# Kernel optimization log

Measured on AMD Instinct MI355X. Metric: run time of the kernel, lower is better.

Reference implementation:

```python
import jax, jax.numpy as jnp
import numpy as np

H = 2048      # hidden_size
K = 16        # n_memory_tokens
NQ = K + 2    # extraction queries (+halt, +value)
NH = 4        # extraction heads
HD = H // NH  # head dim = 512
FFN = 2 * H   # ffn_mult=2
MAXE = 128    # memory buffer capacity (full -> eviction path)
B, S = 4, 4096
EPS = 1e-6


def setup_inputs() -> dict:
    key = jax.random.key(0)
    ks = jax.random.split(key, 20)
    r = lambda i, shape, s=0.02: jax.random.normal(ks[i], shape, jnp.float32) * s
    return {
        "hidden_states": jax.random.normal(ks[0], (B, S, H), jnp.float32),
        "buf_entries": jax.random.normal(ks[1], (MAXE, H), jnp.float32),
        "buf_priorities": jax.random.uniform(ks[2], (MAXE,), jnp.float32),
        "queries": r(3, (NQ, H)),
        "Wq": r(4, (H, H)), "Wk": r(5, (H, H)), "Wv": r(6, (H, H)), "Wo": r(7, (H, H)),
        "ln_w": jnp.ones((H,), jnp.float32),
        "Wgate": r(8, (FFN, H)), "Wup": r(9, (FFN, H)), "Wdown": r(10, (H, FFN)),
        "Wp": r(11, (1, H)), "bp": jnp.full((1,), 0.5, jnp.float32),
        "Wh": r(12, (1, H)), "bh": jnp.full((1,), 1.0, jnp.float32),
        "V1": r(13, (H, 2 * H)), "b1": jnp.zeros((H,), jnp.float32),
        "V2": r(14, (H // 4, H)), "b2": jnp.zeros((H // 4,), jnp.float32),
        "V3": jnp.zeros((1, H // 4), jnp.float32), "b3": jnp.zeros((1,), jnp.float32),
    }


def reference(hidden_states, buf_entries, buf_priorities, queries,
              Wq, Wk, Wv, Wo, ln_w, Wgate, Wup, Wdown,
              Wp, bp, Wh, bh, V1, b1, V2, b2, V3, b3):
    b = hidden_states.shape[0]
    # --- cross-attention: NQ learned queries attend over hidden states ---
    q = (queries @ Wq.T).reshape(NQ, NH, HD)               # queries shared across batch
    k = (hidden_states @ Wk.T).reshape(b, -1, NH, HD)      # (b, s, h, d)
    v = (hidden_states @ Wv.T).reshape(b, -1, NH, HD)
    scores = jnp.einsum('qhd,bshd->bhqs', q, k) / jnp.sqrt(jnp.float32(HD))
    attn = jax.nn.softmax(scores, axis=-1)
    out = jnp.einsum('bhqs,bshd->bqhd', attn, v).reshape(b, NQ, H)
    extracted = out @ Wo.T
    memory_raw = extracted[:, :K]            # (b, K, H)
    confidence_vec = extracted[:, K]         # (b, H)
    value_vec = extracted[:, K + 1]          # (b, H)
    # --- RMSNorm + SwiGLU FFN residual (dropout = identity in eval) ---
    ms = jnp.mean(memory_raw * memory_raw, axis=-1, keepdims=True)
    xn = memory_raw * jax.lax.rsqrt(ms + EPS) * ln_w
    ffn = (jax.nn.silu(xn @ Wgate.T) * (xn @ Wup.T)) @ Wdown.T
    memory = memory_raw + ffn
    # --- heads ---
    priority = jax.nn.sigmoid(memory @ Wp.T + bp)[..., 0]          # (b, K)
    confidence = jax.nn.sigmoid(confidence_vec @ Wh.T + bh)[..., 0]  # (b,)
    value_input = jnp.concatenate([value_vec, hidden_states[:, -1, :]], axis=-1)
    h1 = jax.nn.silu(value_input @ V1.T + b1)
    h2 = jax.nn.silu(h1 @ V2.T + b2)
    value = (h2 @ V3.T + b3)[..., 0]                               # (b,)
    # --- MemoryBuffer.store with full buffer: sequential priority eviction ---
    # (torch loops K times with argmin().item() host syncs; lax.scan preserves
    #  the sequential compare-and-replace semantics in one fused program)
    vecs = jax.lax.stop_gradient(memory[0])     # store detaches; uses batch 0
    pris = jax.lax.stop_gradient(priority[0])

    def step(carry, xp):
        ent, pr = carry
        vec, p = xp
        idx = jnp.argmin(pr)
        take = p > pr[idx]
        ent = ent.at[idx].set(jnp.where(take, vec, ent[idx]))
        pr = pr.at[idx].set(jnp.where(take, p, pr[idx]))
        return (ent, pr), None

    (new_entries, new_priorities), _ = jax.lax.scan(step, (buf_entries, buf_priorities), (vecs, pris))
    return memory, priority, confidence, value, new_entries, new_priorities
```

## Files before the change

### kernel.cpp

```cpp
#include <hip/hip_runtime.h>

#define SS    4096
#define HH    2048
#define NQQ   18
#define QH    72
#define SCALE_F 0.044194173824159216f

#define OUT_MEM     0
#define OUT_PRI     131072
#define OUT_CONF    131136
#define OUT_VAL     131140
#define OUT_ENT     131144
#define OUT_NEWPRI  393288

typedef float  f32x4  __attribute__((ext_vector_type(4)));
typedef __bf16 bf16x8 __attribute__((ext_vector_type(8)));

#define DEVFN static __device__ __forceinline__

DEVFN bf16x8 pack8(f32x4 lo, f32x4 hi){
  bf16x8 r;
  #pragma unroll
  for (int i = 0; i < 4; i++){ r[i] = (__bf16)lo[i]; r[i+4] = (__bf16)hi[i]; }
  return r;
}
DEVFN float siluf(float x){ return x / (1.f + expf(-x)); }
DEVFN float block_sum(float v, float* sb){
  #pragma unroll
  for (int o = 32; o > 0; o >>= 1) v += __shfl_xor(v, o);
  int wid = threadIdx.x >> 6, lane = threadIdx.x & 63;
  if (lane == 0) sb[wid] = v;
  __syncthreads();
  v = sb[0] + sb[1] + sb[2] + sb[3];
  __syncthreads();
  return v;
}

template<int MF, int KC, bool HSEL>
__global__ __launch_bounds__(256) void gemm_bt(
    const __bf16* __restrict__ A, int Kf,
    const float* __restrict__ B0, float* __restrict__ C0,
    const float* __restrict__ B1, float* __restrict__ C1,
    int N)
{
  constexpr int Mp = 16 * MF;
  const int lane = threadIdx.x & 63, w = threadIdx.x >> 6;
  const int n0 = blockIdx.x * 64 + w * 16;
  const int k0 = blockIdx.y * KC * 32;
  const float* B = blockIdx.z ? B1 : B0;
  float* Cp      = blockIdx.z ? C1 : C0;
  const __bf16* aBase = A + (HSEL ? (long)(n0 >> 9) * Mp * Kf : 0)
                          + (long)(lane & 15) * Kf + k0 + 8 * (lane >> 4);
  const float* bBase = B + (long)(n0 + (lane & 15)) * Kf + k0 + 8 * (lane >> 4);
  f32x4 acc[MF];
  #pragma unroll
  for (int m = 0; m < MF; m++) acc[m] = (f32x4)(0.f);
  #pragma unroll 4
  for (int c = 0; c < KC; c++){
    f32x4 lo = *reinterpret_cast<const f32x4*>(bBase + c * 32);
    f32x4 hi = *reinterpret_cast<const f32x4*>(bBase + c * 32 + 4);
    bf16x8 bb = pack8(lo, hi);
    #pragma unroll
    for (int m = 0; m < MF; m++){
      bf16x8 aa = *reinterpret_cast<const bf16x8*>(aBase + (long)m * 16 * Kf + c * 32);
      acc[m] = __builtin_amdgcn_mfma_f32_16x16x32_bf16(aa, bb, acc[m], 0, 0, 0);
    }
  }
  float* cp = Cp + (long)blockIdx.y * Mp * N;
  int row0 = 4 * (lane >> 4), col = n0 + (lane & 15);
  #pragma unroll
  for (int m = 0; m < MF; m++)
    #pragma unroll
    for (int r = 0; r < 4; r++)
      cp[(long)(m * 16 + row0 + r) * N + col] = acc[m][r];
}

template<int MF, int KC>
__global__ __launch_bounds__(256) void gemm_abnat(
    const __bf16* __restrict__ A, long aBatch, int aStride,
    const float* __restrict__ Bn, long bBatch,
    float* __restrict__ Cp, long cBatch,
    int N)
{
  constexpr int Mp = 16 * MF;
  const int lane = threadIdx.x & 63, w = threadIdx.x >> 6;
  const int z = blockIdx.z;
  const int n0 = blockIdx.x * 64 + w * 16;
  const int k0 = blockIdx.y * KC * 32;
  const __bf16* aBase = A + z * aBatch + (long)(lane & 15) * aStride + k0 + 8 * (lane >> 4);
  const float* bBase = Bn + z * bBatch + (long)(k0 + 8 * (lane >> 4)) * N + n0 + (lane & 15);
  f32x4 acc[MF];
  #pragma unroll
  for (int m = 0; m < MF; m++) acc[m] = (f32x4)(0.f);
  #pragma unroll 2
  for (int c = 0; c < KC; c++){
    const float* bp = bBase + (long)c * 32 * N;
    bf16x8 bb;
    #pragma unroll
    for (int j = 0; j < 8; j++) bb[j] = (__bf16)bp[(long)j * N];
    #pragma unroll
    for (int m = 0; m < MF; m++){
      bf16x8 aa = *reinterpret_cast<const bf16x8*>(aBase + (long)m * 16 * aStride + c * 32);
      acc[m] = __builtin_amdgcn_mfma_f32_16x16x32_bf16(aa, bb, acc[m], 0, 0, 0);
    }
  }
  float* cp = Cp + z * cBatch + (long)blockIdx.y * Mp * N;
  int row0 = 4 * (lane >> 4), col = n0 + (lane & 15);
  #pragma unroll
  for (int m = 0; m < MF; m++)
    #pragma unroll
    for (int r = 0; r < 4; r++)
      cp[(long)(m * 16 + row0 + r) * N + col] = acc[m][r];
}

template<int KC>
__global__ __launch_bounds__(256) void gemm_pass1(
    const float* __restrict__ hs, const __bf16* __restrict__ qk,
    float* __restrict__ Sp)
{
  const int lane = threadIdx.x & 63, w = threadIdx.x >> 6;
  const int b = blockIdx.z;
  const int s0 = blockIdx.x * 64 + w * 16;
  const int k0 = blockIdx.y * KC * 32;
  const float* aBase = hs + ((long)b * SS + s0 + (lane & 15)) * HH + k0 + 8 * (lane >> 4);
  const __bf16* bBase = qk + (long)(lane & 15) * HH + k0 + 8 * (lane >> 4);
  f32x4 acc[5];
  #pragma unroll
  for (int n = 0; n < 5; n++) acc[n] = (f32x4)(0.f);
  #pragma unroll 4
  for (int c = 0; c < KC; c++){
    f32x4 lo = *reinterpret_cast<const f32x4*>(aBase + c * 32);
    f32x4 hi = *reinterpret_cast<const f32x4*>(aBase + c * 32 + 4);
    bf16x8 aa = pack8(lo, hi);
    #pragma unroll
    for (int n = 0; n < 5; n++){
      bf16x8 bb = *reinterpret_cast<const bf16x8*>(bBase + (long)n * 16 * HH + c * 32);
      acc[n] = __builtin_amdgcn_mfma_f32_16x16x32_bf16(aa, bb, acc[n], 0, 0, 0);
    }
  }
  float* sp = Sp + ((long)blockIdx.y * 4 + b) * 80 * SS;
  int scol = s0 + 4 * (lane >> 4);
  #pragma unroll
  for (int n = 0; n < 5; n++){
    int qh = n * 16 + (lane & 15);
    *reinterpret_cast<f32x4*>(sp + (long)qh * SS + scol) = acc[n];
  }
}

__global__ void k_prep_qA(const float* __restrict__ queries, __bf16* __restrict__ qA){
  int i = blockIdx.x * 256 + threadIdx.x;
  int r = i >> 11;
  qA[i] = (__bf16)((r < NQQ) ? queries[i] : 0.f);
}
__global__ void k_mkQ2(const float* __restrict__ q_p, __bf16* __restrict__ Q2){
  int i = blockIdx.x * 256 + threadIdx.x;
  int qh = i >> 11, e = i & 2047;
  float v = 0.f;
  if (qh < QH){
    int h = qh / NQQ, qq = qh - h * NQQ;
    if ((e >> 9) == h){
      float s = 0.f;
      #pragma unroll
      for (int y = 0; y < 16; y++) s += q_p[(long)y * 32 * 2048 + qq * 2048 + e];
      v = s * SCALE_F;
    }
  }
  Q2[i] = (__bf16)v;
}
__global__ void k_mkqk(const float* __restrict__ qk_p, __bf16* __restrict__ qk_bf){
  int i = blockIdx.x * 256 + threadIdx.x;
  float s = 0.f;
  #pragma unroll
  for (int y = 0; y < 16; y++) s += qk_p[(long)y * 80 * 2048 + i];
  qk_bf[i] = (__bf16)s;
}
__global__ __launch_bounds__(256) void k_softmax(const float* __restrict__ Sp, __bf16* __restrict__ attn){
  int qh = blockIdx.x, b = blockIdx.y;
  __bf16* arow = attn + ((long)b * 80 + qh) * SS;
  if (qh >= QH){
    #pragma unroll
    for (int it = 0; it < 16; it++) arow[threadIdx.x + 256 * it] = (__bf16)0.f;
    return;
  }
  const float* r0 = Sp + ((long)b * 80 + qh) * SS;
  const long ys = (long)4 * 80 * SS;
  float x[16]; float mx = -1e30f;
  #pragma unroll
  for (int it = 0; it < 16; it++){
    int s = threadIdx.x + 256 * it;
    x[it] = (r0[s] + r0[s + ys]) + (r0[s + 2 * ys] + r0[s + 3 * ys]);
    mx = fmaxf(mx, x[it]);
  }
  __shared__ float sb[8];
  #pragma unroll
  for (int o = 32; o > 0; o >>= 1) mx = fmaxf(mx, __shfl_xor(mx, o));
  int wid = threadIdx.x >> 6, lane = threadIdx.x & 63;
  if (lane == 0) sb[wid] = mx;
  __syncthreads();
  mx = fmaxf(fmaxf(sb[0], sb[1]), fmaxf(sb[2], sb[3]));
  float sum = 0.f;
  #pragma unroll
  for (int it = 0; it < 16; it++){ x[it] = expf(x[it] - mx); sum += x[it]; }
  #pragma unroll
  for (int o = 32; o > 0; o >>= 1) sum += __shfl_xor(sum, o);
  if (lane == 0) sb[4 + wid] = sum;
  __syncthreads();
  sum = sb[4] + sb[5] + sb[6] + sb[7];
  float inv = 1.f / sum;
  #pragma unroll
  for (int it = 0; it < 16; it++) arow[threadIdx.x + 256 * it] = (__bf16)(x[it] * inv);
}
__global__ void k_pack_wv(const float* __restrict__ w_p, __bf16* __restrict__ Apack){
  int i = blockIdx.x * 256 + threadIdx.x;
  int h = i / (80 * 2048);
  int r = (i / 2048) % 80;
  int e = i & 2047;
  float v = 0.f;
  if (r < QH){
    int b = r / NQQ, qq = r - b * NQQ;
    const float* base = w_p + ((long)b * 8 * 80 + (h * NQQ + qq)) * 2048 + e;
    #pragma unroll
    for (int y = 0; y < 8; y++) v += base[(long)y * 80 * 2048];
  }
  Apack[i] = (__bf16)v;
}
__global__ void k_sum_outB(const float* __restrict__ outB_p, __bf16* __restrict__ outB){
  int i = blockIdx.x * 256 + threadIdx.x;
  float s = 0.f;
  #pragma unroll
  for (int y = 0; y < 16; y++) s += outB_p[(long)y * 80 * 2048 + i];
  outB[i] = (__bf16)s;
}
__global__ __launch_bounds__(256) void k_rms(const float* __restrict__ ext_p, const float* __restrict__ ln_w,
                                             const float* __restrict__ hs,
                                             float* __restrict__ extracted, __bf16* __restrict__ xnb,
                                             __bf16* __restrict__ vi){
  int r = blockIdx.x;
  if (r >= 80){
    if (r < 84){
      int b = r - 80;
      const float* src = hs + ((long)b * SS + (SS - 1)) * HH;
      #pragma unroll
      for (int it = 0; it < 8; it++){
        int e = threadIdx.x + 256 * it;
        vi[(long)b * 4096 + 2048 + e] = (__bf16)src[e];
      }
    } else {
      int row = 4 + (r - 84);
      #pragma unroll
      for (int it = 0; it < 16; it++)
        vi[(long)row * 4096 + threadIdx.x + 256 * it] = (__bf16)0.f;
    }
    return;
  }
  float xv[8]; float ss = 0.f;
  #pragma unroll
  for (int it = 0; it < 8; it++){
    int e = threadIdx.x + 256 * it;
    float s = 0.f;
    #pragma unroll
    for (int y = 0; y < 16; y++) s += ext_p[((long)y * 80 + r) * 2048 + e];
    extracted[(long)r * 2048 + e] = s;
    xv[it] = s;
    ss += s * s;
  }
  if (r >= QH) return;
  int b = r / NQQ, qq = r - b * NQQ;
  if (qq < 16){
    __shared__ float sb[4];
    ss = block_sum(ss, sb);
    float inv = 1.f / sqrtf(ss * (1.f / 2048.f) + 1e-6f);
    __bf16* dst = xnb + (long)(b * 16 + qq) * HH;
    #pragma unroll
    for (int it = 0; it < 8; it++){
      int e = threadIdx.x + 256 * it;
      dst[e] = (__bf16)(xv[it] * inv * ln_w[e]);
    }
  } else if (qq == 17){
    #pragma unroll
    for (int it = 0; it < 8; it++){
      int e = threadIdx.x + 256 * it;
      vi[(long)b * 4096 + e] = (__bf16)xv[it];
    }
  }
}
__global__ void k_act(const float* __restrict__ gate_p, const float* __restrict__ up_p,
                      __bf16* __restrict__ hb){
  int i = blockIdx.x * 256 + threadIdx.x;
  float g = 0.f, u = 0.f;
  #pragma unroll
  for (int y = 0; y < 4; y++){
    g += gate_p[(long)y * 64 * 4096 + i];
    u += up_p[(long)y * 64 * 4096 + i];
  }
  hb[i] = (__bf16)(siluf(g) * u);
}
__global__ void k_h1act(const float* __restrict__ h1_p, const float* __restrict__ b1,
                        __bf16* __restrict__ h1s){
  int i = blockIdx.x * 256 + threadIdx.x;
  int r = i >> 11, e = i & 2047;
  float v = 0.f;
  if (r < 4){
    float s = 0.f;
    #pragma unroll
    for (int y = 0; y < 16; y++) s += h1_p[(long)y * 16 * 2048 + i];
    v = siluf(s + b1[e]);
  }
  h1s[i] = (__bf16)v;
}
__global__ __launch_bounds__(256) void k_epilogue(
    const float* __restrict__ extracted, const float* __restrict__ ffn_p,
    const float* __restrict__ h2_p,
    const float* __restrict__ Wp, const float* __restrict__ bp,
    const float* __restrict__ Wh, const float* __restrict__ bh,
    const float* __restrict__ b2, const float* __restrict__ V3, const float* __restrict__ b3,
    float* __restrict__ out)
{
  __shared__ float sb[4];
  int blk = blockIdx.x;
  if (blk < 64){
    int b = blk >> 4, qq = blk & 15;
    const float* ext = extracted + (long)(b * NQQ + qq) * HH;
    float pv = 0.f;
    #pragma unroll
    for (int it = 0; it < 8; it++){
      int e = threadIdx.x + 256 * it;
      float f = 0.f;
      #pragma unroll
      for (int y = 0; y < 8; y++) f += ffn_p[((long)y * 64 + blk) * 2048 + e];
      float m = ext[e] + f;
      out[OUT_MEM + (long)blk * 2048 + e] = m;
      pv += m * Wp[e];
    }
    pv = block_sum(pv, sb);
    if (threadIdx.x == 0) out[OUT_PRI + blk] = 1.f / (1.f + expf(-(pv + bp[0])));
  } else if (blk < 68){
    int b = blk - 64;
    const float* m = extracted + (long)(b * NQQ + 16) * HH;
    float v = 0.f;
    #pragma unroll
    for (int it = 0; it < 8; it++){ int e = threadIdx.x + 256 * it; v += m[e] * Wh[e]; }
    v = block_sum(v, sb);
    if (threadIdx.x == 0) out[OUT_CONF + b] = 1.f / (1.f + expf(-(v + bh[0])));
  } else {
    int b = blk - 68;
    float v = 0.f;
    #pragma unroll
    for (int it = 0; it < 2; it++){
      int j = threadIdx.x + 256 * it;
      float s = 0.f;
      #pragma unroll
      for (int y = 0; y < 16; y++) s += h2_p[(long)y * 16 * 512 + b * 512 + j];
      v += siluf(s + b2[j]) * V3[j];
    }
    v = block_sum(v, sb);
    if (threadIdx.x == 0) out[OUT_VAL + b] = v + b3[0];
  }
}
__global__ void k_scan(const float* __restrict__ buf_pri, const float* __restrict__ out_ro,
                       float* __restrict__ out, int* __restrict__ tw){
  int lane = threadIdx.x;
  float pr0 = buf_pri[lane], pr1 = buf_pri[lane + 64];
  int tw0 = -1, tw1 = -1;
  for (int i = 0; i < 16; i++){
    float p = out_ro[OUT_PRI + i];
    float v; int idx;
    if (pr0 <= pr1){ v = pr0; idx = lane; } else { v = pr1; idx = lane + 64; }
    #pragma unroll
    for (int o = 32; o > 0; o >>= 1){
      float ov = __shfl_xor(v, o);
      int   oi = __shfl_xor(idx, o);
      if (ov < v || (ov == v && oi < idx)){ v = ov; idx = oi; }
    }
    if (p > v){
      if (idx == lane)          { pr0 = p; tw0 = i; }
      else if (idx == lane + 64){ pr1 = p; tw1 = i; }
    }
  }
  out[OUT_NEWPRI + lane]      = pr0;
  out[OUT_NEWPRI + lane + 64] = pr1;
  tw[lane] = tw0; tw[lane + 64] = tw1;
}
__global__ void k_entries(const float* __restrict__ buf_ent, const float* __restrict__ out_ro,
                          const int* __restrict__ tw, float* __restrict__ out){
  int row = blockIdx.x;
  int t = tw[row];
  const f32x4* s = reinterpret_cast<const f32x4*>(
      (t < 0) ? (buf_ent + (long)row * HH) : (out_ro + OUT_MEM + (long)t * HH));
  f32x4* d = reinterpret_cast<f32x4*>(out + OUT_ENT + (long)row * HH);
  #pragma unroll
  for (int i = 0; i < 2; i++) d[threadIdx.x + 256 * i] = s[threadIdx.x + 256 * i];
}

extern "C" void kernel_launch(void* const* d_in, const int* in_sizes, int n_in,
                              void* d_out, int out_size, void* d_ws, size_t ws_size,
                              hipStream_t stream)
{
  const float* hs      = (const float*)d_in[0];
  const float* buf_ent = (const float*)d_in[1];
  const float* buf_pri = (const float*)d_in[2];
  const float* queries = (const float*)d_in[3];
  const float* Wq  = (const float*)d_in[4];
  const float* Wk  = (const float*)d_in[5];
  const float* Wv  = (const float*)d_in[6];
  const float* Wo  = (const float*)d_in[7];
  const float* ln_w= (const float*)d_in[8];
  const float* Wgate=(const float*)d_in[9];
  const float* Wup = (const float*)d_in[10];
  const float* Wdown=(const float*)d_in[11];
  const float* Wp  = (const float*)d_in[12];
  const float* bp  = (const float*)d_in[13];
  const float* Wh  = (const float*)d_in[14];
  const float* bh  = (const float*)d_in[15];
  const float* V1  = (const float*)d_in[16];
  const float* b1  = (const float*)d_in[17];
  const float* V2  = (const float*)d_in[18];
  const float* b2  = (const float*)d_in[19];
  const float* V3  = (const float*)d_in[20];
  const float* b3  = (const float*)d_in[21];
  float* out = (float*)d_out;
  char* ws = (char*)d_ws;

  float* q_p      = (float*)(ws + 0);
  float* qk_p     = (float*)(ws + 0);
  float* scores_p = (float*)(ws + 0);
  float* w_p      = (float*)(ws + 0);
  float* outB_p   = (float*)(ws + 0);
  float* ext_p    = (float*)(ws + 0);
  float* gate_p   = (float*)(ws + 0);
  float* up_p     = (float*)(ws + 4194304);
  float* ffn_p    = (float*)(ws + 0);
  __bf16* qA    = (__bf16*)(ws + 20971520);
  __bf16* Q2    = (__bf16*)(ws + 21102592);
  __bf16* qk_bf = (__bf16*)(ws + 21430272);
  __bf16* attn  = (__bf16*)(ws + 21757952);
  __bf16* Apack = (__bf16*)(ws + 24379392);
  __bf16* outB  = (__bf16*)(ws + 25690112);
  float*  extracted = (float*)(ws + 26017792);
  __bf16* xnb   = (__bf16*)(ws + 26673152);
  __bf16* hb    = (__bf16*)(ws + 26935296);
  __bf16* vi    = (__bf16*)(ws + 27459584);
  __bf16* h1s   = (__bf16*)(ws + 27590656);
  float*  h1_p  = (float*)(ws + 27656192);
  float*  h2_p  = (float*)(ws + 29753344);
  int*    tw    = (int*)  (ws + 30277632);

  k_prep_qA<<<256, 256, 0, stream>>>(queries, qA);
  gemm_bt<2, 4, false><<<dim3(32, 16, 1), 256, 0, stream>>>(qA, 2048, Wq, q_p, Wq, q_p, 2048);
  k_mkQ2<<<640, 256, 0, stream>>>(q_p, Q2);
  gemm_abnat<5, 4><<<dim3(32, 16, 1), 256, 0, stream>>>(Q2, 0, 2048, Wk, 0, qk_p, 0, 2048);
  k_mkqk<<<640, 256, 0, stream>>>(qk_p, qk_bf);
  gemm_pass1<16><<<dim3(64, 4, 4), 256, 0, stream>>>(hs, qk_bf, scores_p);
  k_softmax<<<dim3(80, 4), 256, 0, stream>>>(scores_p, attn);
  gemm_abnat<5, 16><<<dim3(32, 8, 4), 256, 0, stream>>>(attn, 80L * 4096, 4096,
      hs, (long)SS * HH, w_p, 8L * 80 * 2048, 2048);
  k_pack_wv<<<2560, 256, 0, stream>>>(w_p, Apack);
  gemm_bt<5, 4, true><<<dim3(32, 16, 1), 256, 0, stream>>>(Apack, 2048, Wv, outB_p, Wv, outB_p, 2048);
  k_sum_outB<<<640, 256, 0, stream>>>(outB_p, outB);
  gemm_bt<5, 4, false><<<dim3(32, 16, 1), 256, 0, stream>>>(outB, 2048, Wo, ext_p, Wo, ext_p, 2048);
  k_rms<<<96, 256, 0, stream>>>(ext_p, ln_w, hs, extracted, xnb, vi);
  gemm_bt<4, 16, false><<<dim3(64, 4, 2), 256, 0, stream>>>(xnb, 2048, Wgate, gate_p, Wup, up_p, 4096);
  gemm_bt<1, 8, false><<<dim3(32, 16, 1), 256, 0, stream>>>(vi, 4096, V1, h1_p, V1, h1_p, 2048);
  k_act<<<1024, 256, 0, stream>>>(gate_p, up_p, hb);
  k_h1act<<<128, 256, 0, stream>>>(h1_p, b1, h1s);
  gemm_bt<4, 16, false><<<dim3(32, 8, 1), 256, 0, stream>>>(hb, 4096, Wdown, ffn_p, Wdown, ffn_p, 2048);
  gemm_bt<1, 4, false><<<dim3(8, 16, 1), 256, 0, stream>>>(h1s, 2048, V2, h2_p, V2, h2_p, 512);
  k_epilogue<<<72, 256, 0, stream>>>(extracted, ffn_p, h2_p, Wp, bp, Wh, bh, b2, V3, b3, out);
  k_scan<<<1, 64, 0, stream>>>(buf_pri, out, out, tw);
  k_entries<<<128, 256, 0, stream>>>(buf_ent, out, tw, out);
}
```

Measured before the change: 282.2 us.

## Merge independent GEMM launches and fuse small prep, activation and scan kernels

Folds query bf16 conversion and the softmax scale into a dedicated Wq GEMM, and merges the FFN gate/up GEMM with the V1 GEMM, the Down GEMM with the V2 GEMM, and the two activation kernels into single launches using block-index dispatch. The FFN GEMMs also use a smaller K-chunk per block, giving more split-K partial slices, more blocks and more reduction traffic. The buffer scan is redundantly recomputed in every block of the entries copy to remove a separate launch. It trades launch count and tail idle time for extra partial-sum memory traffic and duplicated scan work.

```diff
diff --git a/kernel.cpp b/kernel.cpp
--- a/kernel.cpp
+++ b/kernel.cpp
@@ -37,7 +37,7 @@
 }
 
 template<int MF, int KC, bool HSEL>
-__global__ __launch_bounds__(256) void gemm_bt(
+DEVFN void gemm_bt_body(int bx, int by, bool zsel,
     const __bf16* __restrict__ A, int Kf,
     const float* __restrict__ B0, float* __restrict__ C0,
     const float* __restrict__ B1, float* __restrict__ C1,
@@ -45,10 +45,10 @@
 {
   constexpr int Mp = 16 * MF;
   const int lane = threadIdx.x & 63, w = threadIdx.x >> 6;
-  const int n0 = blockIdx.x * 64 + w * 16;
-  const int k0 = blockIdx.y * KC * 32;
-  const float* B = blockIdx.z ? B1 : B0;
-  float* Cp      = blockIdx.z ? C1 : C0;
+  const int n0 = bx * 64 + w * 16;
+  const int k0 = by * KC * 32;
+  const float* B = zsel ? B1 : B0;
+  float* Cp      = zsel ? C1 : C0;
   const __bf16* aBase = A + (HSEL ? (long)(n0 >> 9) * Mp * Kf : 0)
                           + (long)(lane & 15) * Kf + k0 + 8 * (lane >> 4);
   const float* bBase = B + (long)(n0 + (lane & 15)) * Kf + k0 + 8 * (lane >> 4);
@@ -66,13 +66,21 @@
       acc[m] = __builtin_amdgcn_mfma_f32_16x16x32_bf16(aa, bb, acc[m], 0, 0, 0);
     }
   }
-  float* cp = Cp + (long)blockIdx.y * Mp * N;
+  float* cp = Cp + (long)by * Mp * N;
   int row0 = 4 * (lane >> 4), col = n0 + (lane & 15);
   #pragma unroll
   for (int m = 0; m < MF; m++)
     #pragma unroll
     for (int r = 0; r < 4; r++)
       cp[(long)(m * 16 + row0 + r) * N + col] = acc[m][r];
+}
+template<int MF, int KC, bool HSEL>
+__global__ __launch_bounds__(256) void gemm_bt(
+    const __bf16* __restrict__ A, int Kf,
+    const float* __restrict__ B0, float* __restrict__ C0,
+    const float* __restrict__ B1, float* __restrict__ C1, int N)
+{
+  gemm_bt_body<MF, KC, HSEL>(blockIdx.x, blockIdx.y, blockIdx.z != 0, A, Kf, B0, C0, B1, C1, N);
 }
 
 template<int MF, int KC>
@@ -113,6 +121,45 @@
       cp[(long)(m * 16 + row0 + r) * N + col] = acc[m][r];
 }
 
+__global__ __launch_bounds__(256) void gemm_qA(
+    const float* __restrict__ queries, const float* __restrict__ Wq, float* __restrict__ Cp)
+{
+  const int lane = threadIdx.x & 63, w = threadIdx.x >> 6;
+  const int n0 = blockIdx.x * 64 + w * 16;
+  const int k0 = blockIdx.y * 4 * 32;
+  const int r0 = lane & 15, r1 = r0 + 16;
+  const float f1 = (r1 < NQQ) ? SCALE_F : 0.f;
+  const float* a0 = queries + (long)r0 * HH + k0 + 8 * (lane >> 4);
+  const float* a1 = queries + (long)((r1 < NQQ) ? r1 : 0) * HH + k0 + 8 * (lane >> 4);
+  const float* bBase = Wq + (long)(n0 + r0) * HH + k0 + 8 * (lane >> 4);
+  f32x4 acc[2]; acc[0] = (f32x4)(0.f); acc[1] = (f32x4)(0.f);
+  #pragma unroll
+  for (int c = 0; c < 4; c++){
+    f32x4 blo = *reinterpret_cast<const f32x4*>(bBase + c * 32);
+    f32x4 bhi = *reinterpret_cast<const f32x4*>(bBase + c * 32 + 4);
+    bf16x8 bb = pack8(blo, bhi);
+    f32x4 l0 = *reinterpret_cast<const f32x4*>(a0 + c * 32);
+    f32x4 h0 = *reinterpret_cast<const f32x4*>(a0 + c * 32 + 4);
+    f32x4 l1 = *reinterpret_cast<const f32x4*>(a1 + c * 32);
+    f32x4 h1 = *reinterpret_cast<const f32x4*>(a1 + c * 32 + 4);
+    bf16x8 aa0, aa1;
+    #pragma unroll
+    for (int i = 0; i < 4; i++){
+      aa0[i] = (__bf16)(l0[i] * SCALE_F); aa0[i+4] = (__bf16)(h0[i] * SCALE_F);
+      aa1[i] = (__bf16)(l1[i] * f1);      aa1[i+4] = (__bf16)(h1[i] * f1);
+    }
+    acc[0] = __builtin_amdgcn_mfma_f32_16x16x32_bf16(aa0, bb, acc[0], 0, 0, 0);
+    acc[1] = __builtin_amdgcn_mfma_f32_16x16x32_bf16(aa1, bb, acc[1], 0, 0, 0);
+  }
+  float* cp = Cp + (long)blockIdx.y * 32 * HH;
+  int row0 = 4 * (lane >> 4), col = n0 + r0;
+  #pragma unroll
+  for (int m = 0; m < 2; m++)
+    #pragma unroll
+    for (int r = 0; r < 4; r++)
+      cp[(long)(m * 16 + row0 + r) * HH + col] = acc[m][r];
+}
+
 template<int KC>
 __global__ __launch_bounds__(256) void gemm_pass1(
     const float* __restrict__ hs, const __bf16* __restrict__ qk,
@@ -147,11 +194,61 @@
   }
 }
 
-__global__ void k_prep_qA(const float* __restrict__ queries, __bf16* __restrict__ qA){
-  int i = blockIdx.x * 256 + threadIdx.x;
-  int r = i >> 11;
-  qA[i] = (__bf16)((r < NQQ) ? queries[i] : 0.f);
-}
+__global__ __launch_bounds__(256) void k_ffn1(
+    const __bf16* __restrict__ xnb, const float* __restrict__ Wgate, const float* __restrict__ Wup,
+    float* __restrict__ gate_p, float* __restrict__ up_p,
+    const __bf16* __restrict__ vi, const float* __restrict__ V1, float* __restrict__ h1_p)
+{
+  int bid = blockIdx.x;
+  if (bid < 1024){
+    int z = bid >> 9, rem = bid & 511;
+    gemm_bt_body<4, 8, false>(rem & 63, rem >> 6, z != 0, xnb, 2048, Wgate, gate_p, Wup, up_p, 4096);
+  } else {
+    int t = bid - 1024;
+    gemm_bt_body<1, 8, false>(t & 31, t >> 5, false, vi, 4096, V1, h1_p, V1, h1_p, 2048);
+  }
+}
+__global__ __launch_bounds__(256) void k_ffn2(
+    const __bf16* __restrict__ hb, const float* __restrict__ Wdown, float* __restrict__ ffn_p,
+    const __bf16* __restrict__ h1s, const float* __restrict__ V2, float* __restrict__ h2_p)
+{
+  int bid = blockIdx.x;
+  if (bid < 512){
+    gemm_bt_body<4, 8, false>(bid & 31, bid >> 5, false, hb, 4096, Wdown, ffn_p, Wdown, ffn_p, 2048);
+  } else {
+    int t = bid - 512;
+    gemm_bt_body<1, 4, false>(t & 7, t >> 3, false, h1s, 2048, V2, h2_p, V2, h2_p, 512);
+  }
+}
+__global__ void k_act2(const float* __restrict__ gate_p, const float* __restrict__ up_p,
+                       __bf16* __restrict__ hb,
+                       const float* __restrict__ h1_p, const float* __restrict__ b1,
+                       __bf16* __restrict__ h1s)
+{
+  int bid = blockIdx.x;
+  if (bid < 1024){
+    long i = (long)bid * 256 + threadIdx.x;
+    float g = 0.f, u = 0.f;
+    #pragma unroll
+    for (int y = 0; y < 8; y++){
+      g += gate_p[(long)y * 64 * 4096 + i];
+      u += up_p[(long)y * 64 * 4096 + i];
+    }
+    hb[i] = (__bf16)(siluf(g) * u);
+  } else {
+    int i = (bid - 1024) * 256 + threadIdx.x;
+    int r = i >> 11, e = i & 2047;
+    float v = 0.f;
+    if (r < 4){
+      float s = 0.f;
+      #pragma unroll
+      for (int y = 0; y < 16; y++) s += h1_p[(long)y * 16 * 2048 + i];
+      v = siluf(s + b1[e]);
+    }
+    h1s[i] = (__bf16)v;
+  }
+}
+
 __global__ void k_mkQ2(const float* __restrict__ q_p, __bf16* __restrict__ Q2){
   int i = blockIdx.x * 256 + threadIdx.x;
   int qh = i >> 11, e = i & 2047;
@@ -162,7 +259,7 @@
       float s = 0.f;
       #pragma unroll
       for (int y = 0; y < 16; y++) s += q_p[(long)y * 32 * 2048 + qq * 2048 + e];
-      v = s * SCALE_F;
+      v = s;
     }
   }
   Q2[i] = (__bf16)v;
@@ -284,30 +381,6 @@
     }
   }
 }
-__global__ void k_act(const float* __restrict__ gate_p, const float* __restrict__ up_p,
-                      __bf16* __restrict__ hb){
-  int i = blockIdx.x * 256 + threadIdx.x;
-  float g = 0.f, u = 0.f;
-  #pragma unroll
-  for (int y = 0; y < 4; y++){
-    g += gate_p[(long)y * 64 * 4096 + i];
-    u += up_p[(long)y * 64 * 4096 + i];
-  }
-  hb[i] = (__bf16)(siluf(g) * u);
-}
-__global__ void k_h1act(const float* __restrict__ h1_p, const float* __restrict__ b1,
-                        __bf16* __restrict__ h1s){
-  int i = blockIdx.x * 256 + threadIdx.x;
-  int r = i >> 11, e = i & 2047;
-  float v = 0.f;
-  if (r < 4){
-    float s = 0.f;
-    #pragma unroll
-    for (int y = 0; y < 16; y++) s += h1_p[(long)y * 16 * 2048 + i];
-    v = siluf(s + b1[e]);
-  }
-  h1s[i] = (__bf16)v;
-}
 __global__ __launch_bounds__(256) void k_epilogue(
     const float* __restrict__ extracted, const float* __restrict__ ffn_p,
     const float* __restrict__ h2_p,
@@ -327,7 +400,7 @@
       int e = threadIdx.x + 256 * it;
       float f = 0.f;
       #pragma unroll
-      for (int y = 0; y < 8; y++) f += ffn_p[((long)y * 64 + blk) * 2048 + e];
+      for (int y = 0; y < 16; y++) f += ffn_p[((long)y * 64 + blk) * 2048 + e];
       float m = ext[e] + f;
       out[OUT_MEM + (long)blk * 2048 + e] = m;
       pv += m * Wp[e];
@@ -357,39 +430,42 @@
     if (threadIdx.x == 0) out[OUT_VAL + b] = v + b3[0];
   }
 }
-__global__ void k_scan(const float* __restrict__ buf_pri, const float* __restrict__ out_ro,
-                       float* __restrict__ out, int* __restrict__ tw){
-  int lane = threadIdx.x;
-  float pr0 = buf_pri[lane], pr1 = buf_pri[lane + 64];
-  int tw0 = -1, tw1 = -1;
-  for (int i = 0; i < 16; i++){
-    float p = out_ro[OUT_PRI + i];
-    float v; int idx;
-    if (pr0 <= pr1){ v = pr0; idx = lane; } else { v = pr1; idx = lane + 64; }
-    #pragma unroll
-    for (int o = 32; o > 0; o >>= 1){
-      float ov = __shfl_xor(v, o);
-      int   oi = __shfl_xor(idx, o);
-      if (ov < v || (ov == v && oi < idx)){ v = ov; idx = oi; }
-    }
-    if (p > v){
-      if (idx == lane)          { pr0 = p; tw0 = i; }
-      else if (idx == lane + 64){ pr1 = p; tw1 = i; }
-    }
-  }
-  out[OUT_NEWPRI + lane]      = pr0;
-  out[OUT_NEWPRI + lane + 64] = pr1;
-  tw[lane] = tw0; tw[lane + 64] = tw1;
-}
-__global__ void k_entries(const float* __restrict__ buf_ent, const float* __restrict__ out_ro,
-                          const int* __restrict__ tw, float* __restrict__ out){
-  int row = blockIdx.x;
-  int t = tw[row];
+__global__ void k_scanentries(const float* __restrict__ buf_pri, const float* __restrict__ buf_ent,
+                              float* __restrict__ out){
+  __shared__ int tws;
+  int bid = blockIdx.x, tid = threadIdx.x;
+  if (tid < 64){
+    int lane = tid;
+    float pr0 = buf_pri[lane], pr1 = buf_pri[lane + 64];
+    int tw0 = -1, tw1 = -1;
+    for (int i = 0; i < 16; i++){
+      float pp = out[OUT_PRI + i];
+      float v; int idx;
+      if (pr0 <= pr1){ v = pr0; idx = lane; } else { v = pr1; idx = lane + 64; }
+      #pragma unroll
+      for (int o = 32; o > 0; o >>= 1){
+        float ov = __shfl_xor(v, o);
+        int   oi = __shfl_xor(idx, o);
+        if (ov < v || (ov == v && oi < idx)){ v = ov; idx = oi; }
+      }
+      if (pp > v){
+        if (idx == lane)          { pr0 = pp; tw0 = i; }
+        else if (idx == lane + 64){ pr1 = pp; tw1 = i; }
+      }
+    }
+    if (bid == 0){
+      out[OUT_NEWPRI + lane]      = pr0;
+      out[OUT_NEWPRI + lane + 64] = pr1;
+    }
+    if (lane == (bid & 63)) tws = (bid < 64) ? tw0 : tw1;
+  }
+  __syncthreads();
+  int t = tws;
   const f32x4* s = reinterpret_cast<const f32x4*>(
-      (t < 0) ? (buf_ent + (long)row * HH) : (out_ro + OUT_MEM + (long)t * HH));
-  f32x4* d = reinterpret_cast<f32x4*>(out + OUT_ENT + (long)row * HH);
-  #pragma unroll
-  for (int i = 0; i < 2; i++) d[threadIdx.x + 256 * i] = s[threadIdx.x + 256 * i];
+      (t < 0) ? (buf_ent + (long)bid * HH) : (out + OUT_MEM + (long)t * HH));
+  f32x4* d = reinterpret_cast<f32x4*>(out + OUT_ENT + (long)bid * HH);
+  #pragma unroll
+  for (int i = 0; i < 2; i++) d[tid + 256 * i] = s[tid + 256 * i];
 }
 
 extern "C" void kernel_launch(void* const* d_in, const int* in_sizes, int n_in,
@@ -428,9 +504,8 @@
   float* outB_p   = (float*)(ws + 0);
   float* ext_p    = (float*)(ws + 0);
   float* gate_p   = (float*)(ws + 0);
-  float* up_p     = (float*)(ws + 4194304);
+  float* up_p     = (float*)(ws + 8388608);
   float* ffn_p    = (float*)(ws + 0);
-  __bf16* qA    = (__bf16*)(ws + 20971520);
   __bf16* Q2    = (__bf16*)(ws + 21102592);
   __bf16* qk_bf = (__bf16*)(ws + 21430272);
   __bf16* attn  = (__bf16*)(ws + 21757952);
@@ -443,10 +518,8 @@
   __bf16* h1s   = (__bf16*)(ws + 27590656);
   float*  h1_p  = (float*)(ws + 27656192);
   float*  h2_p  = (float*)(ws + 29753344);
-  int*    tw    = (int*)  (ws + 30277632);
-
-  k_prep_qA<<<256, 256, 0, stream>>>(queries, qA);
-  gemm_bt<2, 4, false><<<dim3(32, 16, 1), 256, 0, stream>>>(qA, 2048, Wq, q_p, Wq, q_p, 2048);
+
+  gemm_qA<<<dim3(32, 16), 256, 0, stream>>>(queries, Wq, q_p);
   k_mkQ2<<<640, 256, 0, stream>>>(q_p, Q2);
   gemm_abnat<5, 4><<<dim3(32, 16, 1), 256, 0, stream>>>(Q2, 0, 2048, Wk, 0, qk_p, 0, 2048);
   k_mkqk<<<640, 256, 0, stream>>>(qk_p, qk_bf);
@@ -459,13 +532,9 @@
   k_sum_outB<<<640, 256, 0, stream>>>(outB_p, outB);
   gemm_bt<5, 4, false><<<dim3(32, 16, 1), 256, 0, stream>>>(outB, 2048, Wo, ext_p, Wo, ext_p, 2048);
   k_rms<<<96, 256, 0, stream>>>(ext_p, ln_w, hs, extracted, xnb, vi);
-  gemm_bt<4, 16, false><<<dim3(64, 4, 2), 256, 0, stream>>>(xnb, 2048, Wgate, gate_p, Wup, up_p, 4096);
-  gemm_bt<1, 8, false><<<dim3(32, 16, 1), 256, 0, stream>>>(vi, 4096, V1, h1_p, V1, h1_p, 2048);
-  k_act<<<1024, 256, 0, stream>>>(gate_p, up_p, hb);
-  k_h1act<<<128, 256, 0, stream>>>(h1_p, b1, h1s);
-  gemm_bt<4, 16, false><<<dim3(32, 8, 1), 256, 0, stream>>>(hb, 4096, Wdown, ffn_p, Wdown, ffn_p, 2048);
-  gemm_bt<1, 4, false><<<dim3(8, 16, 1), 256, 0, stream>>>(h1s, 2048, V2, h2_p, V2, h2_p, 512);
+  k_ffn1<<<1536, 256, 0, stream>>>(xnb, Wgate, Wup, gate_p, up_p, vi, V1, h1_p);
+  k_act2<<<1152, 256, 0, stream>>>(gate_p, up_p, hb, h1_p, b1, h1s);
+  k_ffn2<<<640, 256, 0, stream>>>(hb, Wdown, ffn_p, h1s, V2, h2_p);
   k_epilogue<<<72, 256, 0, stream>>>(extracted, ffn_p, h2_p, Wp, bp, Wh, bh, b2, V3, b3, out);
-  k_scan<<<1, 64, 0, stream>>>(buf_pri, out, out, tw);
-  k_entries<<<128, 256, 0, stream>>>(buf_ent, out, tw, out);
-}
+  k_scanentries<<<128, 256, 0, stream>>>(buf_pri, buf_ent, out);
+}
```

After: 254.6 us, median of 2. 1.11x faster.
